# Optimization experiments

Hardware: AMD Instinct MI355X
Metric: run time of the kernel (lower is better)

The kernel has to match this reference:

```python
import jax, jax.numpy as jnp
import numpy as np

N_H = 896
N_EMB = 300
V_IN = 30000
V_OUT = 30000
B = 64
T_ENC = 40
T_DEC = 40


def gru_cell(x, h, Wih, Whh, bih, bhh):
    # PyTorch GRU cell math
    gi = x @ Wih.T + bih          # [B, 3H]
    gh = h @ Whh.T + bhh          # [B, 3H]
    ir, iz, inn = jnp.split(gi, 3, axis=-1)
    hr, hz, hn = jnp.split(gh, 3, axis=-1)
    r = jax.nn.sigmoid(ir + hr)
    z = jax.nn.sigmoid(iz + hz)
    n = jnp.tanh(inn + r * hn)
    return (1.0 - z) * n + z * h


def run_gru(xs, h0, Wih, Whh, bih, bhh, reverse=False):
    # xs: [T, B, E] -> outputs [T, B, H], final hidden [B, H]
    def step(h, x):
        h2 = gru_cell(x, h, Wih, Whh, bih, bhh)
        return h2, h2
    hT, ys = jax.lax.scan(step, h0, xs, reverse=reverse)
    return ys, hT


def setup_inputs() -> dict:
    key = jax.random.key(0)
    ks = jax.random.split(key, 20)
    s = 0.05
    inp = {
        'x_encoder': jax.random.randint(ks[0], (B, T_ENC), 0, V_IN - 1),
        'x_decoder': jax.random.randint(ks[1], (B, T_DEC), 0, V_OUT - 1),
        'emb_enc': jax.random.normal(ks[2], (V_IN, N_EMB), jnp.float32) * s,
        'Wih_f': jax.random.normal(ks[3], (3 * N_H, N_EMB), jnp.float32) * s,
        'Whh_f': jax.random.normal(ks[4], (3 * N_H, N_H), jnp.float32) * s,
        'bih_f': jnp.zeros((3 * N_H,), jnp.float32),
        'bhh_f': jnp.zeros((3 * N_H,), jnp.float32),
        'Wih_b': jax.random.normal(ks[5], (3 * N_H, N_EMB), jnp.float32) * s,
        'Whh_b': jax.random.normal(ks[6], (3 * N_H, N_H), jnp.float32) * s,
        'bih_b': jnp.zeros((3 * N_H,), jnp.float32),
        'bhh_b': jnp.zeros((3 * N_H,), jnp.float32),
        'emb_dec': jax.random.normal(ks[7], (V_OUT, N_EMB), jnp.float32) * s,
        'Wih_d': jax.random.normal(ks[8], (3 * N_H, N_EMB), jnp.float32) * s,
        'Whh_d': jax.random.normal(ks[9], (3 * N_H, N_H), jnp.float32) * s,
        'bih_d': jnp.zeros((3 * N_H,), jnp.float32),
        'bhh_d': jnp.zeros((3 * N_H,), jnp.float32),
        'fc_W': jax.random.normal(ks[10], (V_OUT, 2 * N_H), jnp.float32) * s,
        'fc_b': jnp.zeros((V_OUT,), jnp.float32),
    }
    return inp


def reference(x_encoder, x_decoder, emb_enc, Wih_f, Whh_f, bih_f, bhh_f,
              Wih_b, Whh_b, bih_b, bhh_b, emb_dec, Wih_d, Whh_d, bih_d,
              bhh_d, fc_W, fc_b):
    Bsz = x_encoder.shape[0]
    h0 = jnp.zeros((Bsz, N_H), jnp.float32)

    # ---- Encoder: bidirectional 1-layer GRU (no padding, full lengths) ----
    xs = emb_enc[x_encoder].transpose(1, 0, 2)          # [Te, B, E]
    y_f, h_f = run_gru(xs, h0, Wih_f, Whh_f, bih_f, bhh_f)
    y_b, h_b = run_gru(xs, h0, Wih_b, Whh_b, bih_b, bhh_b, reverse=True)
    y_enc = (y_f + y_b).transpose(1, 0, 2)              # [B, Te, H] (dirs summed)
    h = h_f + h_b                                       # [B, H]

    # ---- Decoder: per-step GRU + dot-product attention over encoder ----
    xd = emb_dec[x_decoder].transpose(1, 0, 2)          # [Td, B, E]

    def dec_step(h, x):
        h2 = gru_cell(x, h, Wih_d, Whh_d, bih_d, bhh_d)        # [B, H]
        scores = jnp.einsum('bth,bh->bt', y_enc, h2)           # ed_mat
        attn = jax.nn.softmax(scores, axis=1)                  # over Te
        ctx = jnp.einsum('bt,bth->bh', attn, y_enc)            # [B, H]
        logits = jnp.concatenate([h2, ctx], axis=-1) @ fc_W.T + fc_b
        return h2, jax.nn.softmax(logits, axis=-1)

    _, ys = jax.lax.scan(dec_step, h, xd)               # [Td, B, V]
    return ys.transpose(1, 0, 2)                        # [B, Td, V]
```

## Files before the change

### kernel.cpp

```cpp
#include <hip/hip_runtime.h>

#define BB 64
#define TE 40
#define TD 40
#define ED 300
#define EP 320
#define HD 896
#define G3 2688
#define VO 30000
#define VP2 30208
#define KZ 1792
#define KT 28
#define MR 2560
#define NBLK 120
#define NWB 248
#define NTN 118
#define NTILE (NTN * 10)

#define FOFF 0
#define BOFF 56
#define DOFF 112
#define AOFF 168
#define TOFF 232
#define ZOFF 352
#define QOFF 448
#define FSTR 32

typedef __attribute__((ext_vector_type(8))) __bf16 bf16x8;
typedef __attribute__((ext_vector_type(4))) float f32x4;
typedef __attribute__((ext_vector_type(4))) unsigned int u32x4;
typedef __attribute__((ext_vector_type(4))) unsigned short u16x4;

typedef __attribute__((address_space(1))) const void av1c;
typedef __attribute__((address_space(3))) void av3;

__device__ __forceinline__ float sig_(float x)  { return 1.0f / (1.0f + __expf(-x)); }
__device__ __forceinline__ float tanh_(float x) { return 1.0f - 2.0f / (__expf(2.0f * x) + 1.0f); }

__device__ __forceinline__ void gload_lds16(const __bf16* g, __bf16* l) {
    __builtin_amdgcn_global_load_lds((av1c*)g, (av3*)l, 16, 0, 0);
}
__device__ __forceinline__ void gload_lds16_sc(const __bf16* g, __bf16* l) {
    __builtin_amdgcn_global_load_lds((av1c*)g, (av3*)l, 16, 0, 17);
}

__device__ __forceinline__ bf16x8 ld128_sc(const __bf16* p) {
    bf16x8 r;
    asm volatile("global_load_dwordx4 %0, %1, off sc0 sc1" : "=v"(r) : "v"(p));
    return r;
}
__device__ __forceinline__ f32x4 ldf4_sc(const float* p) {
    f32x4 r;
    asm volatile("global_load_dwordx4 %0, %1, off sc0 sc1" : "=v"(r) : "v"(p));
    return r;
}
__device__ __forceinline__ float ldf_sc(const float* p) {
    float r;
    asm volatile("global_load_dword %0, %1, off sc0 sc1" : "=v"(r) : "v"(p));
    return r;
}
__device__ __forceinline__ void vm_wait0() {
    asm volatile("s_waitcnt vmcnt(0)" ::: "memory");
}
__device__ __forceinline__ void stf_sc(float* p, float v) {
    asm volatile("global_store_dword %0, %1, off sc0 sc1" :: "v"(p), "v"(v) : "memory");
}
__device__ __forceinline__ void sth_sc(__bf16* p, float v) {
    unsigned int u = (unsigned int)__builtin_bit_cast(unsigned short, (__bf16)v);
    asm volatile("global_store_short %0, %1, off sc0 sc1" :: "v"(p), "v"(u) : "memory");
}
__device__ __forceinline__ void sti_sc(int* p, int v) {
    asm volatile("global_store_dword %0, %1, off sc0 sc1" :: "v"(p), "v"(v) : "memory");
}
__device__ __forceinline__ void spin_ge(const int* p, int target) {
    int v;
    for (;;) {
        asm volatile("global_load_dword %0, %1, off sc0 sc1\n\ts_waitcnt vmcnt(0)"
                     : "=v"(v) : "v"(p) : "memory");
        if (v >= target) break;
        __builtin_amdgcn_s_sleep(1);
    }
}
__device__ __forceinline__ void spinb(const int* p, int target) {
    for (int it = 0; it < (1 << 20); ++it) {
        int v;
        asm volatile("global_load_dword %0, %1, off sc0 sc1\n\ts_waitcnt vmcnt(0)"
                     : "=v"(v) : "v"(p) : "memory");
        if (v >= target) return;
        __builtin_amdgcn_s_sleep(16);
    }
}

__device__ __forceinline__ size_t hblk(int b, int c) {
    return ((size_t)(c >> 4) * 64 + b) * 16 + (c & 15);
}

__device__ __forceinline__ void stage_w(__bf16* wlds, const float* __restrict__ W, int c0)
{
    const int tid = threadIdx.x;
    for (int ch = tid; ch < 48 * 224; ch += 256) {
        const int lr = ch / 224, c4 = (ch % 224) * 4;
        const int g = lr >> 4, rr = lr & 15;
        const int kk = c4 >> 5, hi = (c4 & 31) >> 3, j = c4 & 7;
        const float4 v = *(const float4*)&W[(size_t)(g * HD + c0 + rr) * HD + c4];
        __bf16* d = &wlds[((g * 28 + kk) * 64 + hi * 16 + rr) * 8 + j];
        d[0] = (__bf16)v.x; d[1] = (__bf16)v.y; d[2] = (__bf16)v.z; d[3] = (__bf16)v.w;
    }
}

struct GiReg { float g0[4], g1[4], g2[4]; };

__device__ __forceinline__ GiReg gi_prefetch(const float* __restrict__ GIt,
                                             int c, int w, int hi)
{
    GiReg r;
#pragma unroll
    for (int rg = 0; rg < 4; ++rg) {
        const float* gp = GIt + (size_t)(16 * w + hi * 4 + rg) * G3 + c;
        r.g0[rg] = gp[0]; r.g1[rg] = gp[HD]; r.g2[rg] = gp[2 * HD];
    }
    return r;
}

__device__ __forceinline__ void gru_step(
    const __bf16* __restrict__ hcurB, const float* __restrict__ hcurF,
    const __bf16* __restrict__ wlds, const GiReg& gi,
    float bh0, float bh1, float bh2,
    float* __restrict__ hnF, __bf16* __restrict__ hnB,
    float* __restrict__ yencD, int tt,
    __bf16* __restrict__ zrow,
    int c0, int lane, int w)
{
    const int r16 = lane & 15, hi = lane >> 4;
    const int c = c0 + r16;
    const int colblk = c0 >> 4;
    const int brow = 16 * w;

    bf16x8 afr[28];
    const __bf16* ap = hcurB + ((size_t)(hi >> 1) * 64 + brow + r16) * 16 + (hi & 1) * 8;
#pragma unroll
    for (int kk = 0; kk < 28; ++kk) afr[kk] = ld128_sc(ap + kk * 2048);
    float hp[4];
#pragma unroll
    for (int rg = 0; rg < 4; ++rg)
        hp[rg] = ldf_sc(hcurF + ((size_t)colblk * 64 + brow + hi * 4 + rg) * 16 + r16);
    vm_wait0();
    __builtin_amdgcn_sched_barrier(0);

    f32x4 a0 = {0.f, 0.f, 0.f, 0.f}, a1 = a0, a2 = a0;
#pragma unroll
    for (int kk = 0; kk < 28; ++kk) {
        const bf16x8 b0 = *(const bf16x8*)&wlds[(kk) * 512 + lane * 8];
        const bf16x8 b1 = *(const bf16x8*)&wlds[(28 + kk) * 512 + lane * 8];
        const bf16x8 b2 = *(const bf16x8*)&wlds[(56 + kk) * 512 + lane * 8];
        a0 = __builtin_amdgcn_mfma_f32_16x16x32_bf16(afr[kk], b0, a0, 0, 0, 0);
        a1 = __builtin_amdgcn_mfma_f32_16x16x32_bf16(afr[kk], b1, a1, 0, 0, 0);
        a2 = __builtin_amdgcn_mfma_f32_16x16x32_bf16(afr[kk], b2, a2, 0, 0, 0);
    }

#pragma unroll
    for (int rg = 0; rg < 4; ++rg) {
        const int b = brow + hi * 4 + rg;
        const float rr = sig_(gi.g0[rg] + a0[rg] + bh0);
        const float zz = sig_(gi.g1[rg] + a1[rg] + bh1);
        const float nn = tanh_(gi.g2[rg] + rr * (a2[rg] + bh2));
        const float hnew = (1.0f - zz) * nn + zz * hp[rg];
        const size_t so = ((size_t)colblk * 64 + b) * 16 + r16;
        stf_sc(hnF + so, hnew);
        sth_sc(hnB + so, hnew);
        if (yencD) stf_sc(yencD + (((size_t)colblk * 64 + b) * TE + tt) * 16 + r16, hnew);
        if (zrow)  sth_sc(zrow + (size_t)b * KZ + c, hnew);
    }
}

__device__ __forceinline__ void attn_step512(
    const float* __restrict__ yencL, float* __restrict__ h2s,
    float* __restrict__ scL, float* __restrict__ attwL,
    const float* __restrict__ h2g, int b, __bf16* __restrict__ zr,
    int* __restrict__ myflag, int* __restrict__ zflag, int postval)
{
    const int tid = threadIdx.x, lane = tid & 63, w = tid >> 6;

    float a0 = 0.f, a1 = 0.f;
    if (tid < HD) a0 = ldf_sc(h2g + hblk(b, tid));
    if (tid + 512 < HD) a1 = ldf_sc(h2g + hblk(b, tid + 512));
    vm_wait0();
    __builtin_amdgcn_sched_barrier(0);
    if (tid < HD) h2s[tid] = a0;
    if (tid + 512 < HD) h2s[tid + 512] = a1;
    __syncthreads();
    if (tid == 0) sti_sc(myflag, postval);

    const float2* h22 = (const float2*)h2s;
    for (int t = w; t < TE; t += 8) {
        const float2* y2 = (const float2*)(yencL + t * HD);
        float p = 0.f;
#pragma unroll
        for (int it = 0; it < HD / 128; ++it) {
            const float2 ya = y2[lane + it * 64];
            const float2 hb2 = h22[lane + it * 64];
            p += ya.x * hb2.x + ya.y * hb2.y;
        }
        p += __shfl_down(p, 32); p += __shfl_down(p, 16); p += __shfl_down(p, 8);
        p += __shfl_down(p, 4);  p += __shfl_down(p, 2);  p += __shfl_down(p, 1);
        if (lane == 0) scL[t] = p;
    }
    __syncthreads();

    float m = scL[0];
    for (int t = 1; t < TE; ++t) m = fmaxf(m, scL[t]);
    float s = 0.f;
    for (int t = 0; t < TE; ++t) s += __expf(scL[t] - m);
    const float inv = 1.0f / s;
    if (tid < TE) attwL[tid] = __expf(scL[tid] - m) * inv;
    __syncthreads();

    for (int c = tid; c < HD; c += 512) {
        float acc = 0.f;
#pragma unroll
        for (int t = 0; t < TE; ++t) acc += attwL[t] * yencL[t * HD + c];
        sth_sc(zr + (size_t)b * KZ + HD + c, acc);
    }
    vm_wait0();
    __syncthreads();
    if (tid == 0) sti_sc(zflag, postval);
}

__global__ __launch_bounds__(512, 1) void recur(
    const float* __restrict__ GIf, const float* __restrict__ GIb,
    const float* __restrict__ GId,
    const float* __restrict__ WhhF, const float* __restrict__ WhhB,
    const float* __restrict__ WhhD,
    const float* __restrict__ bhhF, const float* __restrict__ bhhB,
    const float* __restrict__ bhhD,
    float* __restrict__ heF, __bf16* __restrict__ heB,
    float* __restrict__ hdF, __bf16* __restrict__ hdB,
    float* __restrict__ yenc_f, float* __restrict__ yenc_b,
    __bf16* __restrict__ Zb, int* __restrict__ flags,
    const __bf16* __restrict__ fcW, float* __restrict__ outC,
    const float* __restrict__ fcb)
{
    __shared__ __align__(16) char smem[147456];
    __bf16* wlds  = (__bf16*)smem;
    float*  yencL = (float*)smem;
    float*  h2s   = (float*)(smem + 143360);
    float*  scL   = (float*)(smem + 146944);
    float*  attwL = (float*)(smem + 147136);
    volatile int* shtile = (volatile int*)(smem + 147400);

    const int gid = blockIdx.x;
    const int tid = threadIdx.x;
    const int lane = tid & 63, w = tid >> 6;
    const int r16 = lane & 15, hi = lane >> 4;
    const size_t S = (size_t)BB * HD;

    if (gid < NBLK) {
        float bb0 = 0.f, bb1 = 0.f, bb2 = 0.f;
        GiReg gi;

        if (gid < 112) {
            const int dir = (gid >= 56) ? 1 : 0;
            const int gloc = dir ? gid - 56 : gid;
            const int c0e = gloc * 16;
            const float* GIe  = dir ? GIb : GIf;
            const float* bhhE = dir ? bhhB : bhhF;
            float* yencD = dir ? yenc_b : yenc_f;
            const int foff = dir ? BOFF : FOFF;
            const int ce = c0e + r16;

            stage_w(wlds, dir ? WhhB : WhhF, c0e);
            if (tid < 256) {
                bb0 = bhhE[ce]; bb1 = bhhE[HD + ce]; bb2 = bhhE[2 * HD + ce];
                gi = gi_prefetch(GIe + (size_t)(dir ? TE - 1 : 0) * BB * G3, ce, w, hi);
            }
            __syncthreads();

            for (int t = 0; t < TE; ++t) {
                if (t > 0) {
                    if (tid < 56) spin_ge(flags + (foff + tid) * FSTR, t);
                    __syncthreads();
                }
                const int tt = dir ? (TE - 1 - t) : t;
                if (tid < 256)
                    gru_step(heB + (size_t)(dir * 2 + (t & 1)) * S,
                             heF + (size_t)(dir * 2 + (t & 1)) * S,
                             wlds, gi, bb0, bb1, bb2,
                             heF + (size_t)(dir * 2 + ((t + 1) & 1)) * S,
                             heB + (size_t)(dir * 2 + ((t + 1) & 1)) * S,
                             yencD, tt, nullptr, c0e, lane, w);
                vm_wait0();
                __syncthreads();
                if (tid == 0) sti_sc(flags + (foff + gloc) * FSTR, t + 1);
                if (t + 1 < TE && tid < 256) {
                    const int ttn = dir ? (TE - 2 - t) : (t + 1);
                    gi = gi_prefetch(GIe + (size_t)ttn * BB * G3, ce, w, hi);
                }
            }
        }

        if (tid < 112) spin_ge(flags + tid * FSTR, TE);
        __syncthreads();

        {
            const int i0 = gid * 256 + tid;
            const int i1 = i0 + NBLK * 256;
            const bool has0 = (i0 < BB * HD);
            const bool has1 = (i1 < BB * HD);
            const float f0 = has0 ? ldf_sc(&heF[0 * S + i0]) : 0.f;
            const float b0 = has0 ? ldf_sc(&heF[2 * S + i0]) : 0.f;
            const float f1 = has1 ? ldf_sc(&heF[0 * S + i1]) : 0.f;
            const float b1 = has1 ? ldf_sc(&heF[2 * S + i1]) : 0.f;
            vm_wait0();
            __builtin_amdgcn_sched_barrier(0);
            if (has0) { const float v0 = f0 + b0; stf_sc(&hdF[i0], v0); sth_sc(&hdB[i0], v0); }
            if (has1) { const float v1 = f1 + b1; stf_sc(&hdF[i1], v1); sth_sc(&hdB[i1], v1); }
        }
        if (gid < 56) {
            stage_w(wlds, WhhD, gid * 16);
            if (tid < 256) {
                const int cd = gid * 16 + r16;
                bb0 = bhhD[cd]; bb1 = bhhD[HD + cd]; bb2 = bhhD[2 * HD + cd];
                gi = gi_prefetch(GId, cd, w, hi);
            }
        }
        vm_wait0();
        __syncthreads();
        if (tid == 0) sti_sc(flags + (TOFF + gid) * FSTR, 1);
        if (tid < 120) spin_ge(flags + (TOFF + tid) * FSTR, 1);
        __syncthreads();

        if (gid < 56) {
            for (int p = 0; p < TD; ++p) {
                if (p > 0 && tid < 56) spin_ge(flags + (DOFF + tid) * FSTR, p);
                if (p >= 4 && tid >= 64 && tid < 128)
                    spin_ge(flags + (AOFF + tid - 64) * FSTR, p - 3);
                __syncthreads();
                if (tid < 256)
                    gru_step(hdB + (size_t)(p & 3) * S, hdF + (size_t)(p & 3) * S,
                             wlds, gi, bb0, bb1, bb2,
                             hdF + (size_t)((p + 1) & 3) * S, hdB + (size_t)((p + 1) & 3) * S,
                             nullptr, 0, Zb + (size_t)p * BB * KZ, gid * 16, lane, w);
                vm_wait0();
                __syncthreads();
                if (tid == 0) sti_sc(flags + (DOFF + gid) * FSTR, p + 1);
                if (p + 1 < TD && tid < 256)
                    gi = gi_prefetch(GId + (size_t)(p + 1) * BB * G3, gid * 16 + r16, w, hi);
            }
        } else {
            const int b = gid - 56;
            const float* sf = yenc_f;
            const float* sb = yenc_b;
            for (int it = 0; it < 4; ++it) {
                f32x4 a_[5], b_[5];
                int tt_[5], gg_[5], cc_[5]; bool ok[5];
#pragma unroll
                for (int u = 0; u < 5; ++u) {
                    const int j = it * 2560 + u * 512 + tid;
                    ok[u] = (j < 8960);
                    if (ok[u]) {
                        gg_[u] = j / 160;
                        const int rem = j - gg_[u] * 160;
                        tt_[u] = rem >> 2;
                        cc_[u] = (rem & 3) * 4;
                        const size_t sa = (((size_t)gg_[u] * 64 + b) * TE + tt_[u]) * 16 + cc_[u];
                        a_[u] = ldf4_sc(sf + sa);
                        b_[u] = ldf4_sc(sb + sa);
                    }
                }
                vm_wait0();
                __builtin_amdgcn_sched_barrier(0);
#pragma unroll
                for (int u = 0; u < 5; ++u)
                    if (ok[u])
                        *(f32x4*)&yencL[(size_t)tt_[u] * HD + gg_[u] * 16 + cc_[u]] = a_[u] + b_[u];
            }
            __syncthreads();
            for (int s = 0; s < TD; ++s) {
                if (tid < 56) spin_ge(flags + (DOFF + tid) * FSTR, s + 1);
                __syncthreads();
                attn_step512(yencL, h2s, scL, attwL, hdF + (size_t)((s + 1) & 3) * S,
                             b, Zb + (size_t)s * BB * KZ,
                             flags + (AOFF + b) * FSTR, flags + (ZOFF + b) * FSTR, s + 1);
            }
        }
    }

    {
        __bf16* lds = (__bf16*)smem;
        const int wave = tid >> 6;
        const int wm = wave >> 2, wn = wave & 3;
        int* qcnt = flags + QOFF * FSTR;

        const int srow0 = wave * 8 + (lane >> 3);
        const int scol  = ((lane & 7) ^ (lane >> 3)) * 8;
        const int cbx0 = ((hi * 16) ^ ((r16 & 7) << 4)) >> 1;
        const int cbx1 = ((64 + hi * 16) ^ ((r16 & 7) << 4)) >> 1;

        for (;;) {
            if (tid == 0) {
                const int tl = __hip_atomic_fetch_add(qcnt, 1, __ATOMIC_RELAXED,
                                                      __HIP_MEMORY_SCOPE_AGENT);
                *shtile = tl;
            }
            __syncthreads();
            const int tile = *shtile;
            if (tile >= NTILE) break;
            const int mt = tile / NTN, nt = tile - mt * NTN;
            const int need = 4 * mt + 4;
            if (tid < 56) spinb(flags + (DOFF + tid) * FSTR, need);
            if (tid >= 64 && tid < 128) spinb(flags + (ZOFF + tid - 64) * FSTR, need);
            __syncthreads();

            const long tileM = (long)mt * 256;
            const long tileN = (long)nt * 256;
            const __bf16* gAh[2] = { Zb + (size_t)tileM * KZ, Zb + (size_t)(tileM + 128) * KZ };
            const __bf16* gBh[2] = { fcW + (size_t)tileN * KZ, fcW + (size_t)(tileN + 128) * KZ };
            auto Abase = [](int buf, int h) { return (buf * 2 + h) * 8192; };
            auto Bbase = [](int buf, int h) { return 32768 + (buf * 2 + h) * 8192; };
            auto stageA = [&](const __bf16* gph, int kt, int lbase) {
                const __bf16* g0 = gph + (size_t)srow0 * KZ + kt * 64 + scol;
                gload_lds16_sc(g0, &lds[lbase + wave * 512]);
                gload_lds16_sc(g0 + (size_t)64 * KZ, &lds[lbase + (8 + wave) * 512]);
            };
            auto stageB = [&](const __bf16* gph, int kt, int lbase) {
                const __bf16* g0 = gph + (size_t)srow0 * KZ + kt * 64 + scol;
                gload_lds16(g0, &lds[lbase + wave * 512]);
                gload_lds16(g0 + (size_t)64 * KZ, &lds[lbase + (8 + wave) * 512]);
            };

            f32x4 acc[8][4];
            const f32x4 zero = {0.f, 0.f, 0.f, 0.f};
#pragma unroll
            for (int m = 0; m < 8; ++m)
#pragma unroll
                for (int n = 0; n < 4; ++n) acc[m][n] = zero;

            stageA(gAh[0], 0, Abase(0, 0));
            stageA(gAh[1], 0, Abase(0, 1));
            stageB(gBh[0], 0, Bbase(0, 0));
            stageB(gBh[1], 0, Bbase(0, 1));
            stageB(gBh[0], 1, Bbase(1, 0));
            stageB(gBh[1], 1, Bbase(1, 1));
            asm volatile("s_waitcnt vmcnt(4)" ::: "memory");
            __builtin_amdgcn_s_barrier();

            for (int kt = 0; kt < KT; ++kt) {
                const int buf = kt & 1;
                const int kn1 = (kt + 1 < KT) ? kt + 1 : 0;
                const int kn2 = (kt + 2 < KT) ? kt + 2 : 0;
                const int Ab = Abase(buf, wm);
                const int Bb = Bbase(buf, wn >> 1);
                bf16x8 bfr[4][2];
#pragma unroll
                for (int q = 0; q < 4; ++q) {
                    if (q == 0) {
#pragma unroll
                        for (int n = 0; n < 4; ++n) {
                            const int rowB = (wn & 1) * 64 + n * 16 + r16;
                            bfr[n][0] = *(const bf16x8*)&lds[Bb + rowB * 64 + cbx0];
                            bfr[n][1] = *(const bf16x8*)&lds[Bb + rowB * 64 + cbx1];
                        }
                    }
                    bf16x8 af[2][2];
#pragma unroll
                    for (int mm = 0; mm < 2; ++mm) {
                        const int rowA = (q * 2 + mm) * 16 + r16;
                        af[mm][0] = *(const bf16x8*)&lds[Ab + rowA * 64 + cbx0];
                        af[mm][1] = *(const bf16x8*)&lds[Ab + rowA * 64 + cbx1];
                    }
                    if (q == 0)      stageA(gAh[0], kn1, Abase(buf ^ 1, 0));
                    else if (q == 1) stageA(gAh[1], kn1, Abase(buf ^ 1, 1));
                    else if (q == 2) stageB(gBh[0], kn2, Bbase(buf, 0));
                    else {
                        stageB(gBh[1], kn2, Bbase(buf, 1));
                        asm volatile("s_waitcnt vmcnt(4)" ::: "memory");
                    }
                    __builtin_amdgcn_s_barrier();
                    asm volatile("s_waitcnt lgkmcnt(0)" ::: "memory");
                    __builtin_amdgcn_sched_barrier(0);
                    __builtin_amdgcn_s_setprio(1);
#pragma unroll
                    for (int mm = 0; mm < 2; ++mm)
#pragma unroll
                        for (int n = 0; n < 4; ++n) {
                            acc[q * 2 + mm][n] = __builtin_amdgcn_mfma_f32_16x16x32_bf16(
                                af[mm][0], bfr[n][0], acc[q * 2 + mm][n], 0, 0, 0);
                            acc[q * 2 + mm][n] = __builtin_amdgcn_mfma_f32_16x16x32_bf16(
                                af[mm][1], bfr[n][1], acc[q * 2 + mm][n], 0, 0, 0);
                        }
                    __builtin_amdgcn_s_setprio(0);
                    __builtin_amdgcn_sched_barrier(0);
                    __builtin_amdgcn_s_barrier();
                }
            }
            asm volatile("s_waitcnt vmcnt(0)" ::: "memory");

#pragma unroll
            for (int m = 0; m < 8; ++m) {
#pragma unroll
                for (int n = 0; n < 4; ++n) {
                    const long gcol = tileN + wn * 64 + n * 16 + r16;
                    if (gcol >= VO) continue;
                    const float bv = fcb[gcol];
#pragma unroll
                    for (int rr = 0; rr < 4; ++rr) {
                        const long grow = tileM + wm * 128 + m * 16 + hi * 4 + rr;
                        const long t = grow >> 6, b = grow & 63;
                        outC[(b * TD + t) * VO + gcol] = acc[m][n][rr] + bv;
                    }
                }
            }
            __syncthreads();
        }
    }
}

__global__ __launch_bounds__(256) void gemm_bt(
    const __bf16* __restrict__ A0, const __bf16* __restrict__ B0,
    float* __restrict__ C0, const float* __restrict__ bias0,
    const __bf16* __restrict__ A1, const __bf16* __restrict__ B1,
    float* __restrict__ C1, const float* __restrict__ bias1,
    int M, int N, int K)
{
    constexpr int BM = 128, BN = 128, BK = 32;
    constexpr int FM = 4, FN = 4;

    const __bf16* A = A0; const __bf16* Bp = B0;
    float* C = C0; const float* bias = bias0;
    if (blockIdx.z == 1) { A = A1; Bp = B1; C = C1; bias = bias1; }

    __shared__ __bf16 Ash[2][BM * BK];
    __shared__ __bf16 Bsh[2][BN * BK];

    const int tid  = threadIdx.x;
    const int lane = tid & 63;
    const int wave = tid >> 6;
    const int wr = wave >> 1, wc = wave & 1;

    const int nwg = gridDim.x * gridDim.y;
    const int orig = blockIdx.y * gridDim.x + blockIdx.x;
    const int q = nwg >> 3, r = nwg & 7;
    const int xcd = orig & 7, idx = orig >> 3;
    const int wg = (xcd < r ? xcd * (q + 1) : r * (q + 1) + (xcd - r) * q) + idx;
    const int mtiles = gridDim.y;
    const long tileM = (long)(wg % mtiles) * BM;
    const long tileN = (long)(wg / mtiles) * BN;

    const int r16 = lane & 15;
    const int hi  = lane >> 4;

    f32x4 acc[FM][FN];
    const f32x4 zero = {0.f, 0.f, 0.f, 0.f};
#pragma unroll
    for (int m = 0; m < FM; ++m)
#pragma unroll
        for (int n = 0; n < FN; ++n) acc[m][n] = zero;

    const int srow = wave * 32 + (lane >> 2);
    const int schunk = (lane & 3) * 8;
    const __bf16* gA = A + (size_t)(tileM + srow) * K + schunk;
    const __bf16* gB = Bp + (size_t)(tileN + srow) * K + schunk;
    const size_t kstep16 = (size_t)16 * K;
    const int lofs = (wave * 32) * BK;

#define STAGE_T(k0_, sel_)                                            \
    do {                                                              \
        gload_lds16(gA + (k0_), &Ash[sel_][lofs]);                    \
        gload_lds16(gA + (k0_) + kstep16, &Ash[sel_][lofs + 16 * BK]);\
        gload_lds16(gB + (k0_), &Bsh[sel_][lofs]);                    \
        gload_lds16(gB + (k0_) + kstep16, &Bsh[sel_][lofs + 16 * BK]);\
    } while (0)

    STAGE_T(0, 0);
    int cur = 0;
    for (int k0 = BK; k0 < K; k0 += BK) {
        STAGE_T(k0, cur ^ 1);
        asm volatile("s_waitcnt vmcnt(4)" ::: "memory");
        __builtin_amdgcn_s_barrier();
        __builtin_amdgcn_sched_barrier(0);

        bf16x8 af[FM], bfr[FN];
#pragma unroll
        for (int m = 0; m < FM; ++m)
            af[m] = *(const bf16x8*)&Ash[cur][(wr * 64 + m * 16 + r16) * BK + hi * 8];
#pragma unroll
        for (int n = 0; n < FN; ++n)
            bfr[n] = *(const bf16x8*)&Bsh[cur][(wc * 64 + n * 16 + r16) * BK + hi * 8];
#pragma unroll
        for (int m = 0; m < FM; ++m)
#pragma unroll
            for (int n = 0; n < FN; ++n)
                acc[m][n] = __builtin_amdgcn_mfma_f32_16x16x32_bf16(af[m], bfr[n], acc[m][n], 0, 0, 0);

        __builtin_amdgcn_sched_barrier(0);
        __builtin_amdgcn_s_barrier();
        __builtin_amdgcn_sched_barrier(0);
        cur ^= 1;
    }
    asm volatile("s_waitcnt vmcnt(0)" ::: "memory");
    __builtin_amdgcn_s_barrier();
    __builtin_amdgcn_sched_barrier(0);
    {
        bf16x8 af[FM], bfr[FN];
#pragma unroll
        for (int m = 0; m < FM; ++m)
            af[m] = *(const bf16x8*)&Ash[cur][(wr * 64 + m * 16 + r16) * BK + hi * 8];
#pragma unroll
        for (int n = 0; n < FN; ++n)
            bfr[n] = *(const bf16x8*)&Bsh[cur][(wc * 64 + n * 16 + r16) * BK + hi * 8];
#pragma unroll
        for (int m = 0; m < FM; ++m)
#pragma unroll
            for (int n = 0; n < FN; ++n)
                acc[m][n] = __builtin_amdgcn_mfma_f32_16x16x32_bf16(af[m], bfr[n], acc[m][n], 0, 0, 0);
    }
#undef STAGE_T

#pragma unroll
    for (int m = 0; m < FM; ++m) {
#pragma unroll
        for (int n = 0; n < FN; ++n) {
            const long gcol = tileN + wc * 64 + n * 16 + r16;
            const float bv = bias ? bias[gcol] : 0.0f;
#pragma unroll
            for (int rr = 0; rr < 4; ++rr) {
                const long grow = tileM + wr * 64 + m * 16 + hi * 4 + rr;
                C[grow * N + gcol] = acc[m][n][rr] + bv;
            }
        }
    }
}

__global__ __launch_bounds__(256) void conv_pad(const float* __restrict__ src,
                                                __bf16* __restrict__ dst,
                                                int Rout, int Rin, int Kout, int Kin)
{
    size_t i = (size_t)blockIdx.x * 256 + threadIdx.x;
    const size_t total = (size_t)Rout * Kout;
    const size_t stride = (size_t)gridDim.x * 256;
    for (; i < total; i += stride) {
        int k = (int)(i % Kout);
        int r = (int)(i / Kout);
        float v = (r < Rin && k < Kin) ? src[(size_t)r * Kin + k] : 0.0f;
        dst[i] = (__bf16)v;
    }
}

__global__ __launch_bounds__(256) void conv_fcw(const float* __restrict__ src,
                                                __bf16* __restrict__ dst)
{
    const size_t total4 = (size_t)VP2 * KZ / 4;
    for (size_t i = (size_t)blockIdx.x * 256 + threadIdx.x; i < total4;
         i += (size_t)gridDim.x * 256) {
        const size_t e0 = i * 4;
        const int r = (int)(e0 / KZ);
        u16x4 o;
        if (r < VO) {
            const float4 x = *(const float4*)&src[e0];
            o.x = __builtin_bit_cast(unsigned short, (__bf16)x.x);
            o.y = __builtin_bit_cast(unsigned short, (__bf16)x.y);
            o.z = __builtin_bit_cast(unsigned short, (__bf16)x.z);
            o.w = __builtin_bit_cast(unsigned short, (__bf16)x.w);
        } else {
            o.x = 0; o.y = 0; o.z = 0; o.w = 0;
        }
        *(u16x4*)&dst[e0] = o;
    }
}

__global__ __launch_bounds__(256) void gather_embed(const int* __restrict__ tok,
                                                    const float* __restrict__ emb,
                                                    __bf16* __restrict__ X)
{
    int i = blockIdx.x * 256 + threadIdx.x;
    const int total = TE * BB * EP;
    for (; i < total; i += gridDim.x * 256) {
        int e = i % EP;
        int row = i / EP;
        int t = row >> 6, b = row & 63;
        float v = 0.0f;
        if (e < ED) v = emb[(size_t)tok[b * TE + t] * ED + e];
        X[i] = (__bf16)v;
    }
}

__global__ __launch_bounds__(1024) void softmax_kernel(float* __restrict__ out)
{
    __shared__ float row[VO];
    __shared__ float red[16];
    __shared__ float red2[16];
    const size_t base = (size_t)blockIdx.x * VO;
    const int tid = threadIdx.x;
    const int lane = tid & 63, w = tid >> 6;

    float m = -1e30f;
    for (int ch = tid; ch < VO / 4; ch += 1024) {
        const float4 x = *(const float4*)&out[base + ch * 4];
        *(float4*)&row[ch * 4] = x;
        m = fmaxf(fmaxf(fmaxf(m, x.x), x.y), fmaxf(x.z, x.w));
    }
    m = fmaxf(m, __shfl_down(m, 32)); m = fmaxf(m, __shfl_down(m, 16));
    m = fmaxf(m, __shfl_down(m, 8));  m = fmaxf(m, __shfl_down(m, 4));
    m = fmaxf(m, __shfl_down(m, 2));  m = fmaxf(m, __shfl_down(m, 1));
    if (lane == 0) red[w] = m;
    __syncthreads();
    if (tid == 0) {
        float mm = red[0];
#pragma unroll
        for (int i = 1; i < 16; ++i) mm = fmaxf(mm, red[i]);
        red[0] = mm;
    }
    __syncthreads();
    m = red[0];

    float s = 0.0f;
    for (int v = tid; v < VO; v += 1024) {
        const float e = __expf(row[v] - m);
        row[v] = e;
        s += e;
    }
    s += __shfl_down(s, 32); s += __shfl_down(s, 16); s += __shfl_down(s, 8);
    s += __shfl_down(s, 4);  s += __shfl_down(s, 2);  s += __shfl_down(s, 1);
    if (lane == 0) red2[w] = s;
    __syncthreads();
    if (tid == 0) {
        float ss = red2[0];
#pragma unroll
        for (int i = 1; i < 16; ++i) ss += red2[i];
        red2[0] = ss;
    }
    __syncthreads();
    s = red2[0];

    const float inv = 1.0f / s;
    for (int ch = tid; ch < VO / 4; ch += 1024) {
        float4 x = *(const float4*)&row[ch * 4];
        x.x *= inv; x.y *= inv; x.z *= inv; x.w *= inv;
        *(float4*)&out[base + ch * 4] = x;
    }
}

extern "C" void kernel_launch(void* const* d_in, const int* in_sizes, int n_in,
                              void* d_out, int out_size, void* d_ws, size_t ws_size,
                              hipStream_t stream)
{
    if (n_in < 18) return;
    const int*   x_enc   = (const int*)d_in[0];
    const int*   x_dec   = (const int*)d_in[1];
    const float* emb_enc = (const float*)d_in[2];
    const float* Wih_f   = (const float*)d_in[3];
    const float* Whh_f   = (const float*)d_in[4];
    const float* bih_f   = (const float*)d_in[5];
    const float* bhh_f   = (const float*)d_in[6];
    const float* Wih_b   = (const float*)d_in[7];
    const float* Whh_b   = (const float*)d_in[8];
    const float* bih_b   = (const float*)d_in[9];
    const float* bhh_b   = (const float*)d_in[10];
    const float* emb_dec = (const float*)d_in[11];
    const float* Wih_d   = (const float*)d_in[12];
    const float* Whh_d   = (const float*)d_in[13];
    const float* bih_d   = (const float*)d_in[14];
    const float* bhh_d   = (const float*)d_in[15];
    const float* fc_W    = (const float*)d_in[16];
    const float* fc_b    = (const float*)d_in[17];
    float* out = (float*)d_out;

    size_t off = 0;
    auto alloc = [&](size_t bytes) -> void* {
        void* p = (char*)d_ws + off;
        off = (off + bytes + 255) & ~(size_t)255;
        return p;
    };
    __bf16* fcWb   = (__bf16*)alloc((size_t)VP2 * KZ * 2);
    __bf16* WihFb  = (__bf16*)alloc((size_t)G3 * EP * 2);
    __bf16* WihBb  = (__bf16*)alloc((size_t)G3 * EP * 2);
    __bf16* WihDb  = (__bf16*)alloc((size_t)G3 * EP * 2);
    __bf16* Xe     = (__bf16*)alloc((size_t)MR * EP * 2);
    __bf16* Xd     = (__bf16*)alloc((size_t)MR * EP * 2);
    float*  GIf    = (float*)alloc((size_t)MR * G3 * 4);
    float*  GIb    = (float*)alloc((size_t)MR * G3 * 4);
    float*  GId    = (float*)alloc((size_t)MR * G3 * 4);
    __bf16* Zb     = (__bf16*)alloc((size_t)MR * KZ * 2);
    float*  yenc_f = (float*)alloc((size_t)BB * TE * HD * 4);
    float*  yenc_b = (float*)alloc((size_t)BB * TE * HD * 4);
    float*  hdF    = (float*)alloc((size_t)4 * BB * HD * 4);
    __bf16* hdB    = (__bf16*)alloc((size_t)4 * BB * HD * 2);
    char* zero_start = (char*)d_ws + off;
    float*  heF    = (float*)alloc((size_t)4 * BB * HD * 4);
    __bf16* heB    = (__bf16*)alloc((size_t)4 * BB * HD * 2);
    int*    flags  = (int*)alloc(512 * FSTR * 4);
    size_t zero_bytes = (size_t)(((char*)d_ws + off) - zero_start);
    if (off > ws_size) return;

    hipMemsetAsync(zero_start, 0, zero_bytes, stream);
    conv_fcw<<<8192, 256, 0, stream>>>(fc_W, fcWb);
    conv_pad<<<3360, 256, 0, stream>>>(Wih_f, WihFb, G3, G3, EP, ED);
    conv_pad<<<3360, 256, 0, stream>>>(Wih_b, WihBb, G3, G3, EP, ED);
    conv_pad<<<3360, 256, 0, stream>>>(Wih_d, WihDb, G3, G3, EP, ED);
    gather_embed<<<3200, 256, 0, stream>>>(x_enc, emb_enc, Xe);
    gather_embed<<<3200, 256, 0, stream>>>(x_dec, emb_dec, Xd);

    gemm_bt<<<dim3(G3 / 128, MR / 128, 2), 256, 0, stream>>>(
        Xe, WihFb, GIf, bih_f, Xe, WihBb, GIb, bih_b, MR, G3, EP);
    gemm_bt<<<dim3(G3 / 128, MR / 128, 1), 256, 0, stream>>>(
        Xd, WihDb, GId, bih_d, nullptr, nullptr, nullptr, nullptr, MR, G3, EP);

    recur<<<NWB, 512, 0, stream>>>(GIf, GIb, GId, Whh_f, Whh_b, Whh_d,
                                   bhh_f, bhh_b, bhh_d,
                                   heF, heB, hdF, hdB, yenc_f, yenc_b, Zb, flags,
                                   fcWb, out, fc_b);

    softmax_kernel<<<BB * TD, 1024, 0, stream>>>(out);
}
```

Before: 919.1 us.

## Fuse fc weight conversion and output softmax into persistent recurrence kernel

The separate fc_W bf16 conversion kernel now runs on the otherwise idle non-recurrence blocks (128 slices) while the GRU recurrence executes. Each block signals a counter that gates the vocab GEMM. The standalone row softmax kernel is also folded in. GEMM tiles bump per-M-tile completion counters, and blocks pull softmax rows from an atomic queue once all N tiles of their M-tile are done. This overlaps conversion and softmax with other work and removes kernel launches, at the cost of extra cross-block spin synchronization, cache-bypassing stores and 512-thread softmax blocks.

Result: no change. 915.4 us (-0.4%).

```diff
diff --git a/kernel.cpp b/kernel.cpp
--- a/kernel.cpp
+++ b/kernel.cpp
@@ -24,6 +24,9 @@
 #define TOFF 232
 #define ZOFF 352
 #define QOFF 448
+#define FWC  456
+#define MTO  464
+#define QSO  496
 #define FSTR 32
 
 typedef __attribute__((ext_vector_type(8))) __bf16 bf16x8;
@@ -68,6 +71,9 @@
 __device__ __forceinline__ void sth_sc(__bf16* p, float v) {
     unsigned int u = (unsigned int)__builtin_bit_cast(unsigned short, (__bf16)v);
     asm volatile("global_store_short %0, %1, off sc0 sc1" :: "v"(p), "v"(u) : "memory");
+}
+__device__ __forceinline__ void st8_sc(__bf16* p, u16x4 v) {
+    asm volatile("global_store_dwordx2 %0, %1, off sc0 sc1" :: "v"(p), "v"(v) : "memory");
 }
 __device__ __forceinline__ void sti_sc(int* p, int v) {
     asm volatile("global_store_dword %0, %1, off sc0 sc1" :: "v"(p), "v"(v) : "memory");
@@ -226,6 +232,74 @@
     if (tid == 0) sti_sc(zflag, postval);
 }
 
+__device__ __forceinline__ void softmax512(float* row, float* red, float* red2,
+                                           float* __restrict__ orow)
+{
+    const int tid = threadIdx.x, lane = tid & 63, w = tid >> 6;
+
+    for (int it = 0; it < 3; ++it) {
+        f32x4 v[5]; int jj[5]; bool ok[5];
+#pragma unroll
+        for (int u = 0; u < 5; ++u) {
+            jj[u] = it * 2560 + u * 512 + tid;
+            ok[u] = jj[u] < VO / 4;
+            if (ok[u]) v[u] = ldf4_sc(orow + (size_t)jj[u] * 4);
+        }
+        vm_wait0();
+        __builtin_amdgcn_sched_barrier(0);
+#pragma unroll
+        for (int u = 0; u < 5; ++u)
+            if (ok[u]) *(f32x4*)&row[(size_t)jj[u] * 4] = v[u];
+    }
+    __syncthreads();
+
+    float m = -1e30f;
+    for (int ch = tid; ch < VO / 4; ch += 512) {
+        const f32x4 x = *(const f32x4*)&row[ch * 4];
+        m = fmaxf(fmaxf(fmaxf(m, x[0]), x[1]), fmaxf(x[2], x[3]));
+    }
+    m = fmaxf(m, __shfl_down(m, 32)); m = fmaxf(m, __shfl_down(m, 16));
+    m = fmaxf(m, __shfl_down(m, 8));  m = fmaxf(m, __shfl_down(m, 4));
+    m = fmaxf(m, __shfl_down(m, 2));  m = fmaxf(m, __shfl_down(m, 1));
+    if (lane == 0) red[w] = m;
+    __syncthreads();
+    if (tid == 0) {
+        float mm = red[0];
+#pragma unroll
+        for (int i = 1; i < 8; ++i) mm = fmaxf(mm, red[i]);
+        red[0] = mm;
+    }
+    __syncthreads();
+    m = red[0];
+
+    float s = 0.0f;
+    for (int v2 = tid; v2 < VO; v2 += 512) {
+        const float e = __expf(row[v2] - m);
+        row[v2] = e;
+        s += e;
+    }
+    s += __shfl_down(s, 32); s += __shfl_down(s, 16); s += __shfl_down(s, 8);
+    s += __shfl_down(s, 4);  s += __shfl_down(s, 2);  s += __shfl_down(s, 1);
+    if (lane == 0) red2[w] = s;
+    __syncthreads();
+    if (tid == 0) {
+        float ss = red2[0];
+#pragma unroll
+        for (int i = 1; i < 8; ++i) ss += red2[i];
+        red2[0] = ss;
+    }
+    __syncthreads();
+    s = red2[0];
+
+    const float inv = 1.0f / s;
+    for (int ch = tid; ch < VO / 4; ch += 512) {
+        f32x4 x = *(const f32x4*)&row[ch * 4];
+        x[0] *= inv; x[1] *= inv; x[2] *= inv; x[3] *= inv;
+        *(f32x4*)&orow[(size_t)ch * 4] = x;
+    }
+    __syncthreads();
+}
+
 __global__ __launch_bounds__(512, 1) void recur(
     const float* __restrict__ GIf, const float* __restrict__ GIb,
     const float* __restrict__ GId,
@@ -237,8 +311,8 @@
     float* __restrict__ hdF, __bf16* __restrict__ hdB,
     float* __restrict__ yenc_f, float* __restrict__ yenc_b,
     __bf16* __restrict__ Zb, int* __restrict__ flags,
-    const __bf16* __restrict__ fcW, float* __restrict__ outC,
-    const float* __restrict__ fcb)
+    const float* __restrict__ fcWsrc, __bf16* __restrict__ fcW,
+    float* __restrict__ outC, const float* __restrict__ fcb)
 {
     __shared__ __align__(16) char smem[147456];
     __bf16* wlds  = (__bf16*)smem;
@@ -246,6 +320,8 @@
     float*  h2s   = (float*)(smem + 143360);
     float*  scL   = (float*)(smem + 146944);
     float*  attwL = (float*)(smem + 147136);
+    float*  redA  = (float*)(smem + 131072);
+    float*  redB  = (float*)(smem + 131136);
     volatile int* shtile = (volatile int*)(smem + 147400);
 
     const int gid = blockIdx.x;
@@ -383,6 +459,30 @@
                              flags + (AOFF + b) * FSTR, flags + (ZOFF + b) * FSTR, s + 1);
             }
         }
+    } else {
+        const int slice = gid - NBLK;
+        const size_t base = (size_t)slice * 236 * KZ;
+        const int nf4 = 236 * KZ / 4;
+        for (int i = tid; i < nf4; i += 512) {
+            const size_t e0 = base + (size_t)i * 4;
+            const int r = (int)(e0 / KZ);
+            u16x4 o;
+            if (r < VO) {
+                const float4 x = *(const float4*)&fcWsrc[e0];
+                o.x = __builtin_bit_cast(unsigned short, (__bf16)x.x);
+                o.y = __builtin_bit_cast(unsigned short, (__bf16)x.y);
+                o.z = __builtin_bit_cast(unsigned short, (__bf16)x.z);
+                o.w = __builtin_bit_cast(unsigned short, (__bf16)x.w);
+            } else {
+                o.x = 0; o.y = 0; o.z = 0; o.w = 0;
+            }
+            st8_sc(&fcW[e0], o);
+        }
+        vm_wait0();
+        __syncthreads();
+        if (tid == 0)
+            __hip_atomic_fetch_add(flags + FWC * FSTR, 1, __ATOMIC_RELAXED,
+                                   __HIP_MEMORY_SCOPE_AGENT);
     }
 
     {
@@ -390,6 +490,9 @@
         const int wave = tid >> 6;
         const int wm = wave >> 2, wn = wave & 3;
         int* qcnt = flags + QOFF * FSTR;
+
+        if (tid == 0) spinb(flags + FWC * FSTR, 128);
+        __syncthreads();
 
         const int srow0 = wave * 8 + (lane >> 3);
         const int scol  = ((lane & 7) ^ (lane >> 3)) * 8;
@@ -506,11 +609,36 @@
                     for (int rr = 0; rr < 4; ++rr) {
                         const long grow = tileM + wm * 128 + m * 16 + hi * 4 + rr;
                         const long t = grow >> 6, b = grow & 63;
-                        outC[(b * TD + t) * VO + gcol] = acc[m][n][rr] + bv;
+                        stf_sc(&outC[(b * TD + t) * VO + gcol], acc[m][n][rr] + bv);
                     }
                 }
             }
+            vm_wait0();
             __syncthreads();
+            if (tid == 0)
+                __hip_atomic_fetch_add(flags + (MTO + mt) * FSTR, 1, __ATOMIC_RELAXED,
+                                       __HIP_MEMORY_SCOPE_AGENT);
+            __syncthreads();
+        }
+    }
+
+    {
+        int* qs = flags + QSO * FSTR;
+        for (;;) {
+            if (tid == 0) {
+                const int qv = __hip_atomic_fetch_add(qs, 1, __ATOMIC_RELAXED,
+                                                      __HIP_MEMORY_SCOPE_AGENT);
+                *shtile = qv;
+            }
+            __syncthreads();
+            const int q = *shtile;
+            if (q >= MR) break;
+            const int mt = q >> 8;
+            if (tid == 0) spinb(flags + (MTO + mt) * FSTR, NTN);
+            __syncthreads();
+            const int sub = q & 255;
+            const int t = 4 * mt + (sub >> 6), b = sub & 63;
+            softmax512((float*)smem, redA, redB, outC + (size_t)(b * TD + t) * VO);
         }
     }
 }
@@ -643,28 +771,6 @@
         int r = (int)(i / Kout);
         float v = (r < Rin && k < Kin) ? src[(size_t)r * Kin + k] : 0.0f;
         dst[i] = (__bf16)v;
-    }
-}
-
-__global__ __launch_bounds__(256) void conv_fcw(const float* __restrict__ src,
-                                                __bf16* __restrict__ dst)
-{
-    const size_t total4 = (size_t)VP2 * KZ / 4;
-    for (size_t i = (size_t)blockIdx.x * 256 + threadIdx.x; i < total4;
-         i += (size_t)gridDim.x * 256) {
-        const size_t e0 = i * 4;
-        const int r = (int)(e0 / KZ);
-        u16x4 o;
-        if (r < VO) {
-            const float4 x = *(const float4*)&src[e0];
-            o.x = __builtin_bit_cast(unsigned short, (__bf16)x.x);
-            o.y = __builtin_bit_cast(unsigned short, (__bf16)x.y);
-            o.z = __builtin_bit_cast(unsigned short, (__bf16)x.z);
-            o.w = __builtin_bit_cast(unsigned short, (__bf16)x.w);
-        } else {
-            o.x = 0; o.y = 0; o.z = 0; o.w = 0;
-        }
-        *(u16x4*)&dst[e0] = o;
     }
 }
 
@@ -681,62 +787,6 @@
         float v = 0.0f;
         if (e < ED) v = emb[(size_t)tok[b * TE + t] * ED + e];
         X[i] = (__bf16)v;
-    }
-}
-
-__global__ __launch_bounds__(1024) void softmax_kernel(float* __restrict__ out)
-{
-    __shared__ float row[VO];
-    __shared__ float red[16];
-    __shared__ float red2[16];
-    const size_t base = (size_t)blockIdx.x * VO;
-    const int tid = threadIdx.x;
-    const int lane = tid & 63, w = tid >> 6;
-
-    float m = -1e30f;
-    for (int ch = tid; ch < VO / 4; ch += 1024) {
-        const float4 x = *(const float4*)&out[base + ch * 4];
-        *(float4*)&row[ch * 4] = x;
-        m = fmaxf(fmaxf(fmaxf(m, x.x), x.y), fmaxf(x.z, x.w));
-    }
-    m = fmaxf(m, __shfl_down(m, 32)); m = fmaxf(m, __shfl_down(m, 16));
-    m = fmaxf(m, __shfl_down(m, 8));  m = fmaxf(m, __shfl_down(m, 4));
-    m = fmaxf(m, __shfl_down(m, 2));  m = fmaxf(m, __shfl_down(m, 1));
-    if (lane == 0) red[w] = m;
-    __syncthreads();
-    if (tid == 0) {
-        float mm = red[0];
-#pragma unroll
-        for (int i = 1; i < 16; ++i) mm = fmaxf(mm, red[i]);
-        red[0] = mm;
-    }
-    __syncthreads();
-    m = red[0];
-
-    float s = 0.0f;
-    for (int v = tid; v < VO; v += 1024) {
-        const float e = __expf(row[v] - m);
-        row[v] = e;
-        s += e;
-    }
-    s += __shfl_down(s, 32); s += __shfl_down(s, 16); s += __shfl_down(s, 8);
-    s += __shfl_down(s, 4);  s += __shfl_down(s, 2);  s += __shfl_down(s, 1);
-    if (lane == 0) red2[w] = s;
-    __syncthreads();
-    if (tid == 0) {
-        float ss = red2[0];
-#pragma unroll
-        for (int i = 1; i < 16; ++i) ss += red2[i];
-        red2[0] = ss;
-    }
-    __syncthreads();
-    s = red2[0];
-
-    const float inv = 1.0f / s;
-    for (int ch = tid; ch < VO / 4; ch += 1024) {
-        float4 x = *(const float4*)&row[ch * 4];
-        x.x *= inv; x.y *= inv; x.z *= inv; x.w *= inv;
-        *(float4*)&out[base + ch * 4] = x;
     }
 }
 
@@ -793,7 +843,6 @@
     if (off > ws_size) return;
 
     hipMemsetAsync(zero_start, 0, zero_bytes, stream);
-    conv_fcw<<<8192, 256, 0, stream>>>(fc_W, fcWb);
     conv_pad<<<3360, 256, 0, stream>>>(Wih_f, WihFb, G3, G3, EP, ED);
     conv_pad<<<3360, 256, 0, stream>>>(Wih_b, WihBb, G3, G3, EP, ED);
     conv_pad<<<3360, 256, 0, stream>>>(Wih_d, WihDb, G3, G3, EP, ED);
@@ -808,7 +857,5 @@
     recur<<<NWB, 512, 0, stream>>>(GIf, GIb, GId, Whh_f, Whh_b, Whh_d,
                                    bhh_f, bhh_b, bhh_d,
                                    heF, heB, hdF, hdB, yenc_f, yenc_b, Zb, flags,
-                                   fcWb, out, fc_b);
-
-    softmax_kernel<<<BB * TD, 1024, 0, stream>>>(out);
-}
+                                   fc_W, fcWb, out, fc_b);
+}
```

## Overlap fc_W bf16 conversion with recurrence inside persistent kernel

Applied to the files above, without the earlier changes.

Removes the separate conv_fcw launch and has the 128 otherwise-idle worker blocks of the persistent recur kernel convert fc_W to bf16 while the 120 recurrence blocks run the encoder/decoder. Each converter block handles a 236-row slice and bumps a completion counter, and all blocks wait on that counter before entering the output-GEMM tile loop. This hides the conversion's memory traffic behind the latency-bound recurrence, at the cost of extra bandwidth contention during the recurrence and a new global flag dependency.

Result: faster. 890.9 us (-3.1%).

```diff
diff --git a/kernel.cpp b/kernel.cpp
--- a/kernel.cpp
+++ b/kernel.cpp
@@ -24,6 +24,7 @@
 #define TOFF 232
 #define ZOFF 352
 #define QOFF 448
+#define FWC  456
 #define FSTR 32
 
 typedef __attribute__((ext_vector_type(8))) __bf16 bf16x8;
@@ -68,6 +69,9 @@
 __device__ __forceinline__ void sth_sc(__bf16* p, float v) {
     unsigned int u = (unsigned int)__builtin_bit_cast(unsigned short, (__bf16)v);
     asm volatile("global_store_short %0, %1, off sc0 sc1" :: "v"(p), "v"(u) : "memory");
+}
+__device__ __forceinline__ void st8_sc(__bf16* p, u16x4 v) {
+    asm volatile("global_store_dwordx2 %0, %1, off sc0 sc1" :: "v"(p), "v"(v) : "memory");
 }
 __device__ __forceinline__ void sti_sc(int* p, int v) {
     asm volatile("global_store_dword %0, %1, off sc0 sc1" :: "v"(p), "v"(v) : "memory");
@@ -237,8 +241,8 @@
     float* __restrict__ hdF, __bf16* __restrict__ hdB,
     float* __restrict__ yenc_f, float* __restrict__ yenc_b,
     __bf16* __restrict__ Zb, int* __restrict__ flags,
-    const __bf16* __restrict__ fcW, float* __restrict__ outC,
-    const float* __restrict__ fcb)
+    const float* __restrict__ fcWsrc, __bf16* __restrict__ fcW,
+    float* __restrict__ outC, const float* __restrict__ fcb)
 {
     __shared__ __align__(16) char smem[147456];
     __bf16* wlds  = (__bf16*)smem;
@@ -383,6 +387,30 @@
                              flags + (AOFF + b) * FSTR, flags + (ZOFF + b) * FSTR, s + 1);
             }
         }
+    } else {
+        const int slice = gid - NBLK;
+        const size_t base = (size_t)slice * 236 * KZ;
+        const int nf4 = 236 * KZ / 4;
+        for (int i = tid; i < nf4; i += 512) {
+            const size_t e0 = base + (size_t)i * 4;
+            const int r = (int)(e0 / KZ);
+            u16x4 o;
+            if (r < VO) {
+                const float4 x = *(const float4*)&fcWsrc[e0];
+                o.x = __builtin_bit_cast(unsigned short, (__bf16)x.x);
+                o.y = __builtin_bit_cast(unsigned short, (__bf16)x.y);
+                o.z = __builtin_bit_cast(unsigned short, (__bf16)x.z);
+                o.w = __builtin_bit_cast(unsigned short, (__bf16)x.w);
+            } else {
+                o.x = 0; o.y = 0; o.z = 0; o.w = 0;
+            }
+            st8_sc(&fcW[e0], o);
+        }
+        vm_wait0();
+        __syncthreads();
+        if (tid == 0)
+            __hip_atomic_fetch_add(flags + FWC * FSTR, 1, __ATOMIC_RELAXED,
+                                   __HIP_MEMORY_SCOPE_AGENT);
     }
 
     {
@@ -390,6 +418,9 @@
         const int wave = tid >> 6;
         const int wm = wave >> 2, wn = wave & 3;
         int* qcnt = flags + QOFF * FSTR;
+
+        if (tid == 0) spinb(flags + FWC * FSTR, 128);
+        __syncthreads();
 
         const int srow0 = wave * 8 + (lane >> 3);
         const int scol  = ((lane & 7) ^ (lane >> 3)) * 8;
@@ -643,28 +674,6 @@
         int r = (int)(i / Kout);
         float v = (r < Rin && k < Kin) ? src[(size_t)r * Kin + k] : 0.0f;
         dst[i] = (__bf16)v;
-    }
-}
-
-__global__ __launch_bounds__(256) void conv_fcw(const float* __restrict__ src,
-                                                __bf16* __restrict__ dst)
-{
-    const size_t total4 = (size_t)VP2 * KZ / 4;
-    for (size_t i = (size_t)blockIdx.x * 256 + threadIdx.x; i < total4;
-         i += (size_t)gridDim.x * 256) {
-        const size_t e0 = i * 4;
-        const int r = (int)(e0 / KZ);
-        u16x4 o;
-        if (r < VO) {
-            const float4 x = *(const float4*)&src[e0];
-            o.x = __builtin_bit_cast(unsigned short, (__bf16)x.x);
-            o.y = __builtin_bit_cast(unsigned short, (__bf16)x.y);
-            o.z = __builtin_bit_cast(unsigned short, (__bf16)x.z);
-            o.w = __builtin_bit_cast(unsigned short, (__bf16)x.w);
-        } else {
-            o.x = 0; o.y = 0; o.z = 0; o.w = 0;
-        }
-        *(u16x4*)&dst[e0] = o;
     }
 }
 
@@ -793,7 +802,6 @@
     if (off > ws_size) return;
 
     hipMemsetAsync(zero_start, 0, zero_bytes, stream);
-    conv_fcw<<<8192, 256, 0, stream>>>(fc_W, fcWb);
     conv_pad<<<3360, 256, 0, stream>>>(Wih_f, WihFb, G3, G3, EP, ED);
     conv_pad<<<3360, 256, 0, stream>>>(Wih_b, WihBb, G3, G3, EP, ED);
     conv_pad<<<3360, 256, 0, stream>>>(Wih_d, WihDb, G3, G3, EP, ED);
@@ -808,7 +816,7 @@
     recur<<<NWB, 512, 0, stream>>>(GIf, GIb, GId, Whh_f, Whh_b, Whh_d,
                                    bhh_f, bhh_b, bhh_d,
                                    heF, heB, hdF, hdB, yenc_f, yenc_b, Zb, flags,
-                                   fcWb, out, fc_b);
+                                   fc_W, fcWb, out, fc_b);
 
     softmax_kernel<<<BB * TD, 1024, 0, stream>>>(out);
 }
```
